# Optimization experiments

Hardware: AMD Instinct MI355X
Metric: run time of the kernel (lower is better)

Reference implementation:

```python
import jax, jax.numpy as jnp
import numpy as np

B, P, D = 256, 256, 514          # batch, num_patches (16^2), model_dim
H, HD = 8, 64                    # n_heads, head_dim ((D-2)//H)
SH = 256                         # shared_hidden = head_mlp_hidden_dims[0]
HH = 256                         # per-head hidden (head_mlp_hidden_dims[1])
DFF = 2048                       # ffn hidden
LH = 2 * SH                      # lat_modulator hidden = shared_hidden*2
LD = D - 2                       # learnable_dim

def gelu(x):
    return jax.nn.gelu(x, approximate=False)  # torch nn.GELU default is exact erf

def setup_inputs() -> dict:
    key = jax.random.key(0)
    ks = jax.random.split(key, 16)
    s = 0.02
    x = jax.random.normal(ks[0], (B, P, D), dtype=jnp.float32)
    # shared spatial layer: Linear(P -> SH), torch weight layout [out, in]
    Ws = jax.random.normal(ks[1], (SH, P), dtype=jnp.float32) * s
    bs = jax.random.normal(ks[2], (SH,), dtype=jnp.float32) * s
    # lat modulator: Linear(2 -> LH), GELU, Linear(LH -> 2*SH) with special init
    LW1 = jax.random.normal(ks[3], (LH, 2), dtype=jnp.float32) * s
    Lb1 = jax.random.normal(ks[4], (LH,), dtype=jnp.float32) * s
    LW2 = jnp.zeros((2 * SH, LH), dtype=jnp.float32)  # zeroed per module init
    Lb2 = jnp.concatenate([jnp.ones((SH,), jnp.float32), jnp.zeros((SH,), jnp.float32)])
    # per-head processing: Linear(SH->HH), GELU, Linear(HH->P), stacked over heads
    HW1 = jax.random.normal(ks[5], (H, HH, SH), dtype=jnp.float32) * s
    Hb1 = jax.random.normal(ks[6], (H, HH), dtype=jnp.float32) * s
    HW2 = jax.random.normal(ks[7], (H, P, HH), dtype=jnp.float32) * s
    Hb2 = jax.random.normal(ks[8], (H, P), dtype=jnp.float32) * s
    # ffn: Linear(D -> DFF) with last-2 input cols zeroed, GELU, Linear(DFF -> LD)
    FW1 = jax.random.normal(ks[9], (DFF, D), dtype=jnp.float32) * s
    FW1 = FW1.at[:, -2:].set(0.0)
    Fb1 = jax.random.normal(ks[10], (DFF,), dtype=jnp.float32) * s
    FW2 = jax.random.normal(ks[11], (LD, DFF), dtype=jnp.float32) * s
    Fb2 = jax.random.normal(ks[12], (LD,), dtype=jnp.float32) * s
    return dict(x=x, Ws=Ws, bs=bs, LW1=LW1, Lb1=Lb1, LW2=LW2, Lb2=Lb2,
                HW1=HW1, Hb1=Hb1, HW2=HW2, Hb2=Hb2,
                FW1=FW1, Fb1=Fb1, FW2=FW2, Fb2=Fb2)

def reference(x, Ws, bs, LW1, Lb1, LW2, Lb2, HW1, Hb1, HW2, Hb2, FW1, Fb1, FW2, Fb2):
    central = P // 2
    sc_central = x[:, central, -2:]          # [B, 2]
    sc_all = x[:, :, -2:]                    # [B, P, 2]
    x_learn = x[:, :, :-2]                   # [B, P, LD]
    x_res = x_learn
    # all heads at once: [B, P, H, HD] -> [B, H, HD, P]
    xh = x_learn.reshape(B, P, H, HD).transpose(0, 2, 3, 1)
    shared = jnp.einsum('bhdp,op->bhdo', xh, Ws) + bs   # [B, H, HD, SH]
    # FiLM params (loop-invariant in original, hoisted here)
    mod = gelu(sc_central @ LW1.T + Lb1) @ LW2.T + Lb2  # [B, 2*SH]
    gamma = mod[:, :SH][:, None, None, :]
    beta = mod[:, SH:][:, None, None, :]
    shared = shared * gamma + beta
    # per-head MLPs as grouped GEMMs
    h = gelu(jnp.einsum('bhdo,hko->bhdk', shared, HW1) + Hb1[None, :, None, :])
    out = jnp.einsum('bhdk,hpk->bhdp', h, HW2) + Hb2[None, :, None, :]  # [B,H,HD,P]
    x_learn = out.transpose(0, 3, 1, 2).reshape(B, P, LD) + x_res
    x_full = jnp.concatenate([x_learn, sc_all], axis=-1)  # [B, P, D]
    f = gelu(x_full @ FW1.T + Fb1) @ FW2.T + Fb2          # [B, P, LD]
    x_learn = f + x_learn
    return jnp.concatenate([x_learn, sc_all], axis=-1)
```

## Files before the change

kernel.cpp:

```cpp
#include <hip/hip_runtime.h>
#include <math.h>

typedef __attribute__((ext_vector_type(8))) __bf16 bf16x8;
typedef __attribute__((ext_vector_type(4))) float f32x4;
typedef __attribute__((ext_vector_type(2))) float f32x2;

#define DEV __device__ __forceinline__

typedef __attribute__((address_space(3))) unsigned int lds_u32;
typedef __attribute__((address_space(1))) unsigned int glb_u32;

DEV unsigned short f2bf(float f) {
    unsigned int u = __builtin_bit_cast(unsigned int, f);
    u += 0x7FFFu + ((u >> 16) & 1u);
    return (unsigned short)(u >> 16);
}
DEV float bf2f(unsigned short u) {
    unsigned int v = (unsigned int)u << 16;
    return __builtin_bit_cast(float, v);
}
DEV unsigned int pack2(float a, float b) {
    return (unsigned int)f2bf(a) | ((unsigned int)f2bf(b) << 16);
}
DEV float gelu_exact(float v) {
    return 0.5f * v * (1.0f + erff(v * 0.70710678118654752f));
}
DEV float gelu_fast(float x) {
    float z = 1.5957691216f * x + 0.0713548163f * x * x * x;
    float e = __expf(-z);
    return x * __builtin_amdgcn_rcpf(1.0f + e);
}

__global__ void cast_bf16_kernel(const float* __restrict__ src,
                                 unsigned short* __restrict__ dst, int n) {
    int i = blockIdx.x * 256 + threadIdx.x;
    if (i < n) dst[i] = f2bf(src[i]);
}

__global__ void cast_fw1_kernel(const float* __restrict__ src,
                                unsigned short* __restrict__ dst) {
    int i = blockIdx.x * 256 + threadIdx.x;
    if (i < 2048 * 512) {
        int row = i >> 9, k = i & 511;
        dst[i] = f2bf(src[row * 514 + k]);
    }
}

__global__ void gb_kernel(const float* __restrict__ x,
                          const float* __restrict__ LW1, const float* __restrict__ Lb1,
                          const float* __restrict__ LW2, const float* __restrict__ Lb2,
                          float* __restrict__ gb) {
    __shared__ float t[8][512];
    const int b0 = blockIdx.x * 8, tid = threadIdx.x;
    for (int idx = tid; idx < 8 * 512; idx += 256) {
        int bb = idx >> 9, j = idx & 511;
        float s0 = x[((size_t)(b0 + bb) * 256 + 128) * 514 + 512];
        float s1 = x[((size_t)(b0 + bb) * 256 + 128) * 514 + 513];
        t[bb][j] = gelu_exact(LW1[j * 2] * s0 + LW1[j * 2 + 1] * s1 + Lb1[j]);
    }
    __syncthreads();
    const int i = tid;
    float a0[8], a1[8];
    float l0 = Lb2[i], l1 = Lb2[i + 256];
    #pragma unroll
    for (int bb = 0; bb < 8; ++bb) { a0[bb] = l0; a1[bb] = l1; }
    for (int j = 0; j < 512; ++j) {
        float w0 = LW2[(size_t)i * 512 + j];
        float w1 = LW2[(size_t)(i + 256) * 512 + j];
        #pragma unroll
        for (int bb = 0; bb < 8; ++bb) {
            a0[bb] += w0 * t[bb][j];
            a1[bb] += w1 * t[bb][j];
        }
    }
    #pragma unroll
    for (int bb = 0; bb < 8; ++bb) {
        gb[(size_t)(b0 + bb) * 512 + i] = a0[bb];
        gb[(size_t)(b0 + bb) * 512 + i + 256] = a1[bb];
    }
}

__global__ void sc_copy_kernel(const float* __restrict__ x, float* __restrict__ out,
                               float* __restrict__ scbuf) {
    size_t idx = (size_t)blockIdx.x * 256 + threadIdx.x;
    size_t off = idx * 514 + 512;
    f32x2 v = *(const f32x2*)(x + off);
    *(f32x2*)(out + off) = v;
    *(f32x2*)(scbuf + idx * 2) = v;
}

#define MPAD 264

__global__ __launch_bounds__(256, 2) void mixer_kernel(
    const float* __restrict__ x, const float* __restrict__ bs,
    const float* __restrict__ Hb1, const float* __restrict__ Hb2,
    const unsigned short* __restrict__ Wsb,
    const unsigned short* __restrict__ HW1b,
    const unsigned short* __restrict__ HW2b,
    const float* __restrict__ gb,
    float* __restrict__ out,
    unsigned short* __restrict__ Xb) {
    __shared__ __attribute__((aligned(16))) char smem[33792 + 34816];
    unsigned short* XT = (unsigned short*)smem;
    unsigned short* S = (unsigned short*)(smem + 33792);
    unsigned short* ST = S;

    const int bid = blockIdx.x;
    const int b = bid >> 3;
    const int h = bid & 7;
    const int tid = threadIdx.x;
    const int lane = tid & 63;
    const int w = tid >> 6;
    const int l15 = lane & 15;
    const int l4 = lane >> 4;

    {
        const int c = lane;
        const float* xp = x + ((size_t)b * 256) * 514 + (size_t)h * 64 + c;
        for (int i = 0; i < 32; ++i) {
            int p = (i * 4 + w) * 2;
            float v0 = xp[(size_t)p * 514];
            float v1 = xp[(size_t)(p + 1) * 514];
            *(unsigned int*)&XT[c * MPAD + p] = pack2(v0, v1);
        }
    }
    __syncthreads();

    f32x4 acc[4][4];

    #pragma unroll
    for (int mt = 0; mt < 4; ++mt)
        #pragma unroll
        for (int nt = 0; nt < 4; ++nt) acc[mt][nt] = 0.f;
    {
        bf16x8 bnx[4];
        #pragma unroll
        for (int nt = 0; nt < 4; ++nt)
            bnx[nt] = *(const bf16x8*)(Wsb + (size_t)(w * 64 + nt * 16 + l15) * 256 + l4 * 8);
        for (int kc = 0; kc < 8; ++kc) {
            bf16x8 bcur[4];
            #pragma unroll
            for (int nt = 0; nt < 4; ++nt) bcur[nt] = bnx[nt];
            if (kc < 7) {
                #pragma unroll
                for (int nt = 0; nt < 4; ++nt)
                    bnx[nt] = *(const bf16x8*)(Wsb + (size_t)(w * 64 + nt * 16 + l15) * 256 + (kc + 1) * 32 + l4 * 8);
            }
            #pragma unroll
            for (int mt = 0; mt < 4; ++mt) {
                bf16x8 afr = *(const bf16x8*)&XT[(mt * 16 + l15) * MPAD + kc * 32 + l4 * 8];
                #pragma unroll
                for (int nt = 0; nt < 4; ++nt)
                    acc[mt][nt] = __builtin_amdgcn_mfma_f32_16x16x32_bf16(afr, bcur[nt], acc[mt][nt], 0, 0, 0);
            }
        }
    }
    #pragma unroll
    for (int nt = 0; nt < 4; ++nt) {
        int o = w * 64 + nt * 16 + l15;
        float bsv = bs[o];
        float g = gb[(size_t)b * 512 + o];
        float be = gb[(size_t)b * 512 + 256 + o];
        #pragma unroll
        for (int mt = 0; mt < 4; ++mt)
            #pragma unroll
            for (int r = 0; r < 4; ++r) {
                int c = mt * 16 + l4 * 4 + r;
                S[c * MPAD + o] = f2bf((acc[mt][nt][r] + bsv) * g + be);
            }
    }
    __syncthreads();

    const unsigned short* W2p = HW1b + (size_t)h * 65536;
    #pragma unroll
    for (int mt = 0; mt < 4; ++mt)
        #pragma unroll
        for (int nt = 0; nt < 4; ++nt) acc[mt][nt] = 0.f;
    {
        bf16x8 bnx[4];
        #pragma unroll
        for (int nt = 0; nt < 4; ++nt)
            bnx[nt] = *(const bf16x8*)(W2p + (size_t)(w * 64 + nt * 16 + l15) * 256 + l4 * 8);
        for (int kc = 0; kc < 8; ++kc) {
            bf16x8 bcur[4];
            #pragma unroll
            for (int nt = 0; nt < 4; ++nt) bcur[nt] = bnx[nt];
            if (kc < 7) {
                #pragma unroll
                for (int nt = 0; nt < 4; ++nt)
                    bnx[nt] = *(const bf16x8*)(W2p + (size_t)(w * 64 + nt * 16 + l15) * 256 + (kc + 1) * 32 + l4 * 8);
            }
            #pragma unroll
            for (int mt = 0; mt < 4; ++mt) {
                bf16x8 afr = *(const bf16x8*)&S[(mt * 16 + l15) * MPAD + kc * 32 + l4 * 8];
                #pragma unroll
                for (int nt = 0; nt < 4; ++nt)
                    acc[mt][nt] = __builtin_amdgcn_mfma_f32_16x16x32_bf16(afr, bcur[nt], acc[mt][nt], 0, 0, 0);
            }
        }
    }
    #pragma unroll
    for (int nt = 0; nt < 4; ++nt) {
        int kk = w * 64 + nt * 16 + l15;
        float hb = Hb1[(size_t)h * 256 + kk];
        #pragma unroll
        for (int mt = 0; mt < 4; ++mt)
            #pragma unroll
            for (int r = 0; r < 4; ++r) {
                int c = mt * 16 + l4 * 4 + r;
                XT[c * MPAD + kk] = f2bf(gelu_fast(acc[mt][nt][r] + hb));
            }
    }
    __syncthreads();

    const unsigned short* W3p = HW2b + (size_t)h * 65536;
    #pragma unroll
    for (int mt = 0; mt < 4; ++mt)
        #pragma unroll
        for (int nt = 0; nt < 4; ++nt) acc[mt][nt] = 0.f;
    {
        bf16x8 bnx[4];
        #pragma unroll
        for (int nt = 0; nt < 4; ++nt)
            bnx[nt] = *(const bf16x8*)(W3p + (size_t)(w * 64 + nt * 16 + l15) * 256 + l4 * 8);
        for (int kc = 0; kc < 8; ++kc) {
            bf16x8 bcur[4];
            #pragma unroll
            for (int nt = 0; nt < 4; ++nt) bcur[nt] = bnx[nt];
            if (kc < 7) {
                #pragma unroll
                for (int nt = 0; nt < 4; ++nt)
                    bnx[nt] = *(const bf16x8*)(W3p + (size_t)(w * 64 + nt * 16 + l15) * 256 + (kc + 1) * 32 + l4 * 8);
            }
            #pragma unroll
            for (int mt = 0; mt < 4; ++mt) {
                bf16x8 afr = *(const bf16x8*)&XT[(mt * 16 + l15) * MPAD + kc * 32 + l4 * 8];
                #pragma unroll
                for (int nt = 0; nt < 4; ++nt)
                    acc[mt][nt] = __builtin_amdgcn_mfma_f32_16x16x32_bf16(afr, bcur[nt], acc[mt][nt], 0, 0, 0);
            }
        }
    }
    #pragma unroll
    for (int nt = 0; nt < 4; ++nt) {
        int p = w * 64 + nt * 16 + l15;
        float hb = Hb2[(size_t)h * 256 + p];
        #pragma unroll
        for (int mt = 0; mt < 4; ++mt) {
            ushort4 uv;
            uv.x = f2bf(acc[mt][nt][0] + hb);
            uv.y = f2bf(acc[mt][nt][1] + hb);
            uv.z = f2bf(acc[mt][nt][2] + hb);
            uv.w = f2bf(acc[mt][nt][3] + hb);
            *(ushort4*)(ST + p * 68 + mt * 16 + l4 * 4) = uv;
        }
    }
    __syncthreads();

    #pragma unroll
    for (int s = 0; s < 16; ++s) {
        int row = s * 16 + w * 4 + l4;
        ushort4 u = *(const ushort4*)(ST + row * 68 + l15 * 4);
        const float* xr = x + ((size_t)(b * 256 + row)) * 514 + h * 64 + l15 * 4;
        f32x2 xa = *(const f32x2*)xr;
        f32x2 xc = *(const f32x2*)(xr + 2);
        float o0 = bf2f(u.x) + xa.x;
        float o1 = bf2f(u.y) + xa.y;
        float o2 = bf2f(u.z) + xc.x;
        float o3 = bf2f(u.w) + xc.y;
        float* orow = out + ((size_t)(b * 256 + row)) * 514 + h * 64 + l15 * 4;
        f32x2 w0; w0.x = o0; w0.y = o1;
        f32x2 w1; w1.x = o2; w1.y = o3;
        *(f32x2*)orow = w0;
        *(f32x2*)(orow + 2) = w1;
        ushort4 xo;
        xo.x = f2bf(o0); xo.y = f2bf(o1); xo.z = f2bf(o2); xo.w = f2bf(o3);
        *(ushort4*)(Xb + ((size_t)(b * 256 + row)) * 512 + h * 64 + l15 * 4) = xo;
    }
}

DEV void stage_half(const unsigned short* g, size_t gstride, int row0, int k0,
                    char* half_base, int w, int lane) {
    const int slot = lane & 7;
    const int r8 = lane >> 3;
    const int swz = (slot ^ r8) * 16;
    #pragma unroll
    for (int i = 0; i < 2; ++i) {
        int chunk = w * 2 + i;
        int row = chunk * 8 + r8;
        const char* src = (const char*)(g + (size_t)(row0 + row) * gstride + k0) + swz;
        __builtin_amdgcn_global_load_lds((const glb_u32*)src,
                                         (lds_u32*)(half_base + chunk * 1024), 16, 0, 0);
    }
}

DEV void gemm8_loop(const unsigned short* A, size_t sA,
                    const unsigned short* B, size_t sB,
                    int m0, int n0, int NT,
                    char* A0, char* A1, char* B0, char* B1,
                    int w, int lane, int l15, int l4,
                    f32x4 (&acc)[2][16]) {
    stage_half(A, sA, m0, 0, A0, w, lane);
    stage_half(A, sA, m0 + 128, 0, A0 + 16384, w, lane);
    stage_half(B, sB, n0, 0, B0, w, lane);
    stage_half(B, sB, n0 + 128, 0, B0 + 16384, w, lane);
    asm volatile("s_waitcnt vmcnt(2)" ::: "memory");
    __builtin_amdgcn_s_barrier();
    __builtin_amdgcn_sched_barrier(0);

    for (int t = 0; t < NT; ++t) {
        const char* Ac = (t & 1) ? A1 : A0;
        const char* Bc = (t & 1) ? B1 : B0;
        char* An = (t & 1) ? A0 : A1;
        char* Bn = (t & 1) ? B0 : B1;
        const int kn = (t + 1) * 64;
        const bool more = (t + 1 < NT);
        const bool last = (t == NT - 1);
        #pragma unroll
        for (int q = 0; q < 4; ++q) {
            bf16x8 af[2][2], bf[2][4];
            #pragma unroll
            for (int kk = 0; kk < 2; ++kk) {
                #pragma unroll
                for (int mt = 0; mt < 2; ++mt) {
                    int row = w * 32 + mt * 16 + l15;
                    af[kk][mt] = *(const bf16x8*)(Ac + row * 128 + ((kk * 64 + l4 * 16) ^ ((row & 7) << 4)));
                }
                #pragma unroll
                for (int nt = 0; nt < 4; ++nt) {
                    int row = q * 64 + nt * 16 + l15;
                    bf[kk][nt] = *(const bf16x8*)(Bc + row * 128 + ((kk * 64 + l4 * 16) ^ ((row & 7) << 4)));
                }
            }
            if (more) {
                if (q == 0) stage_half(A, sA, m0, kn, An, w, lane);
                if (q == 1) stage_half(A, sA, m0 + 128, kn, An + 16384, w, lane);
                if (q == 2) stage_half(B, sB, n0, kn, Bn, w, lane);
                if (q == 3) stage_half(B, sB, n0 + 128, kn, Bn + 16384, w, lane);
            }
            if (q == 1) {
                if (last) asm volatile("s_waitcnt vmcnt(0)" ::: "memory");
                else      asm volatile("s_waitcnt vmcnt(4)" ::: "memory");
            }
            if (q == 3) asm volatile("s_waitcnt vmcnt(2)" ::: "memory");
            __builtin_amdgcn_s_barrier();
            __builtin_amdgcn_sched_barrier(0);
            __builtin_amdgcn_s_setprio(1);
            #pragma unroll
            for (int kk = 0; kk < 2; ++kk)
                #pragma unroll
                for (int mt = 0; mt < 2; ++mt)
                    #pragma unroll
                    for (int nt = 0; nt < 4; ++nt)
                        acc[mt][q * 4 + nt] = __builtin_amdgcn_mfma_f32_16x16x32_bf16(
                            af[kk][mt], bf[kk][nt], acc[mt][q * 4 + nt], 0, 0, 0);
            __builtin_amdgcn_s_setprio(0);
            __builtin_amdgcn_sched_barrier(0);
            __builtin_amdgcn_s_barrier();
        }
    }
}

__global__ __launch_bounds__(512, 1) void gemm1_kernel(
    const unsigned short* __restrict__ A,
    const unsigned short* __restrict__ B,
    const float* __restrict__ Fb1,
    const float* __restrict__ FW1,
    const float* __restrict__ scbuf,
    long pass_m0,
    unsigned short* __restrict__ G) {
    __shared__ __attribute__((aligned(16))) char smem[131072];

    const int nwg = gridDim.x;
    const int cpx = nwg >> 3;
    const int bid = (blockIdx.x & 7) * cpx + (blockIdx.x >> 3);
    const int m0 = (bid >> 3) * 256;
    const int n0 = (bid & 7) * 256;
    const int tid = threadIdx.x;
    const int lane = tid & 63;
    const int w = tid >> 6;
    const int l15 = lane & 15;
    const int l4 = lane >> 4;

    f32x4 acc[2][16];
    #pragma unroll
    for (int mt = 0; mt < 2; ++mt)
        #pragma unroll
        for (int nt = 0; nt < 16; ++nt) acc[mt][nt] = 0.f;

    gemm8_loop(A, 512, B, 512, m0, n0, 8,
               smem, smem + 32768, smem + 65536, smem + 98304,
               w, lane, l15, l4, acc);

    f32x2 scp[2][4];
    #pragma unroll
    for (int mt = 0; mt < 2; ++mt)
        #pragma unroll
        for (int r = 0; r < 4; ++r) {
            long rowg = pass_m0 + m0 + w * 32 + mt * 16 + l4 * 4 + r;
            scp[mt][r] = *(const f32x2*)(scbuf + rowg * 2);
        }
    #pragma unroll
    for (int ntg = 0; ntg < 16; ++ntg) {
        int n = n0 + ntg * 16 + l15;
        float fb = Fb1[n];
        float w512 = FW1[(size_t)n * 514 + 512];
        float w513 = FW1[(size_t)n * 514 + 513];
        #pragma unroll
        for (int mt = 0; mt < 2; ++mt)
            #pragma unroll
            for (int r = 0; r < 4; ++r) {
                long row = m0 + w * 32 + mt * 16 + l4 * 4 + r;
                float v = acc[mt][ntg][r] + fb + scp[mt][r].x * w512 + scp[mt][r].y * w513;
                G[row * 2048 + n] = f2bf(gelu_fast(v));
            }
    }
}

__global__ __launch_bounds__(512, 1) void gemm2_kernel(
    const unsigned short* __restrict__ A,
    const unsigned short* __restrict__ B,
    const float* __restrict__ Fb2,
    long pass_m0,
    float* __restrict__ io) {
    __shared__ __attribute__((aligned(16))) char smem[131072];

    const int nwg = gridDim.x;
    const int cpx = nwg >> 3;
    const int bid = (blockIdx.x & 7) * cpx + (blockIdx.x >> 3);
    const int m0 = (bid >> 1) * 256;
    const int n0 = (bid & 1) * 256;
    const int tid = threadIdx.x;
    const int lane = tid & 63;
    const int w = tid >> 6;
    const int l15 = lane & 15;
    const int l4 = lane >> 4;

    f32x4 acc[2][16];
    #pragma unroll
    for (int mt = 0; mt < 2; ++mt)
        #pragma unroll
        for (int nt = 0; nt < 16; ++nt) acc[mt][nt] = 0.f;

    gemm8_loop(A, 2048, B, 2048, m0, n0, 32,
               smem, smem + 32768, smem + 65536, smem + 98304,
               w, lane, l15, l4, acc);

    #pragma unroll
    for (int ntg = 0; ntg < 16; ++ntg) {
        int n = n0 + ntg * 16 + l15;
        float fb = Fb2[n];
        #pragma unroll
        for (int mt = 0; mt < 2; ++mt)
            #pragma unroll
            for (int r = 0; r < 4; ++r) {
                long rowg = pass_m0 + m0 + w * 32 + mt * 16 + l4 * 4 + r;
                float* p = io + rowg * 514 + n;
                *p = acc[mt][ntg][r] + fb + *p;
            }
    }
}

extern "C" void kernel_launch(void* const* d_in, const int* in_sizes, int n_in,
                              void* d_out, int out_size, void* d_ws, size_t ws_size,
                              hipStream_t stream) {
    const float* x = (const float*)d_in[0];
    const float* Ws = (const float*)d_in[1];
    const float* bs = (const float*)d_in[2];
    const float* LW1 = (const float*)d_in[3];
    const float* Lb1 = (const float*)d_in[4];
    const float* LW2 = (const float*)d_in[5];
    const float* Lb2 = (const float*)d_in[6];
    const float* HW1 = (const float*)d_in[7];
    const float* Hb1 = (const float*)d_in[8];
    const float* HW2 = (const float*)d_in[9];
    const float* Hb2 = (const float*)d_in[10];
    const float* FW1 = (const float*)d_in[11];
    const float* Fb1 = (const float*)d_in[12];
    const float* FW2 = (const float*)d_in[13];
    const float* Fb2 = (const float*)d_in[14];
    float* out = (float*)d_out;

    char* ws = (char*)d_ws;
    unsigned short* Wsb = (unsigned short*)(ws);
    unsigned short* HW1b = (unsigned short*)(ws + 131072);
    unsigned short* HW2b = (unsigned short*)(ws + 1179648);
    unsigned short* FW1b = (unsigned short*)(ws + 2228224);
    unsigned short* FW2b = (unsigned short*)(ws + 4325376);
    float* gb = (float*)(ws + 6422528);
    float* scbuf = (float*)(ws + 6946816);
    unsigned short* Xb = (unsigned short*)(ws + 7471104);
    unsigned short* Gbuf = (unsigned short*)(ws + 7471104 + 67108864);

    const size_t fixed = 7471104 + 67108864;
    int npass = 32;
    for (int np = 1; np <= 32; np *= 2) {
        if (fixed + (size_t)268435456 / np <= ws_size) { npass = np; break; }
    }
    const long Mtot = 65536;
    const long Mp = Mtot / npass;

    cast_bf16_kernel<<<256, 256, 0, stream>>>(Ws, Wsb, 65536);
    cast_bf16_kernel<<<2048, 256, 0, stream>>>(HW1, HW1b, 524288);
    cast_bf16_kernel<<<2048, 256, 0, stream>>>(HW2, HW2b, 524288);
    cast_bf16_kernel<<<4096, 256, 0, stream>>>(FW2, FW2b, 1048576);
    cast_fw1_kernel<<<4096, 256, 0, stream>>>(FW1, FW1b);
    gb_kernel<<<32, 256, 0, stream>>>(x, LW1, Lb1, LW2, Lb2, gb);
    sc_copy_kernel<<<256, 256, 0, stream>>>(x, out, scbuf);

    mixer_kernel<<<2048, 256, 0, stream>>>(x, bs, Hb1, Hb2, Wsb, HW1b, HW2b, gb, out, Xb);

    for (int p = 0; p < npass; ++p) {
        long m0 = (long)p * Mp;
        gemm1_kernel<<<(int)(Mp / 256) * 8, 512, 0, stream>>>(
            Xb + m0 * 512, FW1b, Fb1, FW1, scbuf, m0, Gbuf);
        gemm2_kernel<<<(int)(Mp / 256) * 2, 512, 0, stream>>>(
            Gbuf, FW2b, Fb2, m0, out);
    }
}
```

Baseline: 665.1 us.

## Restructure FFN GEMM warp tiling to 2x4 layout with LDS-staged epilogue

Replaces the 8x1 warp layout (each warp 32 rows by 256 cols) with a 2x4 layout (each warp 128 rows by 64 cols). This raises register reuse of the A and B fragments and uses one barrier per k-tile instead of four. Staging of the next tile is issued at the start of each tile, followed by a full vmcnt wait. The gemm1 epilogue now writes GELU outputs to LDS and stores coalesced 16-byte rows to G instead of scattered 2-byte stores. The host now forces at least two passes, trading some launch overhead for a smaller G buffer footprint, possibly for L2/MALL locality.

```diff
diff --git a/kernel.cpp b/kernel.cpp
--- a/kernel.cpp
+++ b/kernel.cpp
@@ -294,70 +294,75 @@
     }
 }
 
-DEV void gemm8_loop(const unsigned short* A, size_t sA,
-                    const unsigned short* B, size_t sB,
-                    int m0, int n0, int NT,
-                    char* A0, char* A1, char* B0, char* B1,
-                    int w, int lane, int l15, int l4,
-                    f32x4 (&acc)[2][16]) {
-    stage_half(A, sA, m0, 0, A0, w, lane);
-    stage_half(A, sA, m0 + 128, 0, A0 + 16384, w, lane);
-    stage_half(B, sB, n0, 0, B0, w, lane);
-    stage_half(B, sB, n0 + 128, 0, B0 + 16384, w, lane);
-    asm volatile("s_waitcnt vmcnt(2)" ::: "memory");
+DEV void stage4(const unsigned short* A, size_t sA, int m0,
+                const unsigned short* B, size_t sB, int n0, int k0,
+                char* Abuf, char* Bbuf, int w, int lane) {
+    stage_half(A, sA, m0, k0, Abuf, w, lane);
+    stage_half(A, sA, m0 + 128, k0, Abuf + 16384, w, lane);
+    stage_half(B, sB, n0, k0, Bbuf, w, lane);
+    stage_half(B, sB, n0 + 128, k0, Bbuf + 16384, w, lane);
+}
+
+DEV void tile_body(const unsigned short* A, size_t sA, int m0,
+                   const unsigned short* B, size_t sB, int n0,
+                   char* smem, int cb, int kn, bool more,
+                   int vA0, int vA1, int vB0, int vB1,
+                   int w, int lane, f32x4 (&acc)[8][4]) {
+    if (more) {
+        int nb = 32768 - cb;
+        stage4(A, sA, m0, B, sB, n0, kn, smem + nb, smem + 65536 + nb, w, lane);
+    }
+    __builtin_amdgcn_s_setprio(1);
+    #pragma unroll
+    for (int kk = 0; kk < 2; ++kk) {
+        const int vA = kk ? vA1 : vA0;
+        const int vB = kk ? vB1 : vB0;
+        bf16x8 bf[4];
+        #pragma unroll
+        for (int nf = 0; nf < 4; ++nf)
+            bf[nf] = *(const bf16x8*)(smem + vB + cb + nf * 2048);
+        #pragma unroll
+        for (int mh = 0; mh < 2; ++mh) {
+            bf16x8 af[4];
+            #pragma unroll
+            for (int mf = 0; mf < 4; ++mf)
+                af[mf] = *(const bf16x8*)(smem + vA + cb + mh * 8192 + mf * 2048);
+            #pragma unroll
+            for (int mf = 0; mf < 4; ++mf)
+                #pragma unroll
+                for (int nf = 0; nf < 4; ++nf)
+                    acc[mh * 4 + mf][nf] = __builtin_amdgcn_mfma_f32_16x16x32_bf16(
+                        af[mf], bf[nf], acc[mh * 4 + mf][nf], 0, 0, 0);
+        }
+    }
+    __builtin_amdgcn_s_setprio(0);
+    if (more) asm volatile("s_waitcnt vmcnt(0)" ::: "memory");
     __builtin_amdgcn_s_barrier();
-    __builtin_amdgcn_sched_barrier(0);
-
-    for (int t = 0; t < NT; ++t) {
-        const char* Ac = (t & 1) ? A1 : A0;
-        const char* Bc = (t & 1) ? B1 : B0;
-        char* An = (t & 1) ? A0 : A1;
-        char* Bn = (t & 1) ? B0 : B1;
-        const int kn = (t + 1) * 64;
-        const bool more = (t + 1 < NT);
-        const bool last = (t == NT - 1);
-        #pragma unroll
-        for (int q = 0; q < 4; ++q) {
-            bf16x8 af[2][2], bf[2][4];
-            #pragma unroll
-            for (int kk = 0; kk < 2; ++kk) {
-                #pragma unroll
-                for (int mt = 0; mt < 2; ++mt) {
-                    int row = w * 32 + mt * 16 + l15;
-                    af[kk][mt] = *(const bf16x8*)(Ac + row * 128 + ((kk * 64 + l4 * 16) ^ ((row & 7) << 4)));
-                }
-                #pragma unroll
-                for (int nt = 0; nt < 4; ++nt) {
-                    int row = q * 64 + nt * 16 + l15;
-                    bf[kk][nt] = *(const bf16x8*)(Bc + row * 128 + ((kk * 64 + l4 * 16) ^ ((row & 7) << 4)));
-                }
-            }
-            if (more) {
-                if (q == 0) stage_half(A, sA, m0, kn, An, w, lane);
-                if (q == 1) stage_half(A, sA, m0 + 128, kn, An + 16384, w, lane);
-                if (q == 2) stage_half(B, sB, n0, kn, Bn, w, lane);
-                if (q == 3) stage_half(B, sB, n0 + 128, kn, Bn + 16384, w, lane);
-            }
-            if (q == 1) {
-                if (last) asm volatile("s_waitcnt vmcnt(0)" ::: "memory");
-                else      asm volatile("s_waitcnt vmcnt(4)" ::: "memory");
-            }
-            if (q == 3) asm volatile("s_waitcnt vmcnt(2)" ::: "memory");
-            __builtin_amdgcn_s_barrier();
-            __builtin_amdgcn_sched_barrier(0);
-            __builtin_amdgcn_s_setprio(1);
-            #pragma unroll
-            for (int kk = 0; kk < 2; ++kk)
-                #pragma unroll
-                for (int mt = 0; mt < 2; ++mt)
-                    #pragma unroll
-                    for (int nt = 0; nt < 4; ++nt)
-                        acc[mt][q * 4 + nt] = __builtin_amdgcn_mfma_f32_16x16x32_bf16(
-                            af[kk][mt], bf[kk][nt], acc[mt][q * 4 + nt], 0, 0, 0);
-            __builtin_amdgcn_s_setprio(0);
-            __builtin_amdgcn_sched_barrier(0);
-            __builtin_amdgcn_s_barrier();
-        }
+}
+
+DEV void gemm_loop(const unsigned short* A, size_t sA,
+                   const unsigned short* B, size_t sB,
+                   int m0, int n0, int NT,
+                   char* smem, int w, int lane, f32x4 (&acc)[8][4]) {
+    const int wm = w >> 2, wn = w & 3;
+    const int l15 = lane & 15, l4 = lane >> 4;
+    const int sw = (l15 & 7) << 4;
+    const int k0off = (l4 * 16) ^ sw;
+    const int k1off = (64 + l4 * 16) ^ sw;
+    const int aBase = (wm * 128 + l15) * 128;
+    const int bBase = 65536 + (wn * 64 + l15) * 128;
+    const int vA0 = aBase + k0off, vA1 = aBase + k1off;
+    const int vB0 = bBase + k0off, vB1 = bBase + k1off;
+
+    stage4(A, sA, m0, B, sB, n0, 0, smem, smem + 65536, w, lane);
+    asm volatile("s_waitcnt vmcnt(0)" ::: "memory");
+    __builtin_amdgcn_s_barrier();
+
+    for (int t = 0; t < NT; t += 2) {
+        tile_body(A, sA, m0, B, sB, n0, smem, 0, (t + 1) * 64, t + 1 < NT,
+                  vA0, vA1, vB0, vB1, w, lane, acc);
+        tile_body(A, sA, m0, B, sB, n0, smem, 32768, (t + 2) * 64, t + 2 < NT,
+                  vA0, vA1, vB0, vB1, w, lane, acc);
     }
 }
 
@@ -381,39 +386,57 @@
     const int w = tid >> 6;
     const int l15 = lane & 15;
     const int l4 = lane >> 4;
-
-    f32x4 acc[2][16];
-    #pragma unroll
-    for (int mt = 0; mt < 2; ++mt)
-        #pragma unroll
-        for (int nt = 0; nt < 16; ++nt) acc[mt][nt] = 0.f;
-
-    gemm8_loop(A, 512, B, 512, m0, n0, 8,
-               smem, smem + 32768, smem + 65536, smem + 98304,
-               w, lane, l15, l4, acc);
-
-    f32x2 scp[2][4];
-    #pragma unroll
-    for (int mt = 0; mt < 2; ++mt)
-        #pragma unroll
-        for (int r = 0; r < 4; ++r) {
-            long rowg = pass_m0 + m0 + w * 32 + mt * 16 + l4 * 4 + r;
-            scp[mt][r] = *(const f32x2*)(scbuf + rowg * 2);
-        }
-    #pragma unroll
-    for (int ntg = 0; ntg < 16; ++ntg) {
-        int n = n0 + ntg * 16 + l15;
-        float fb = Fb1[n];
-        float w512 = FW1[(size_t)n * 514 + 512];
-        float w513 = FW1[(size_t)n * 514 + 513];
-        #pragma unroll
-        for (int mt = 0; mt < 2; ++mt)
-            #pragma unroll
-            for (int r = 0; r < 4; ++r) {
-                long row = m0 + w * 32 + mt * 16 + l4 * 4 + r;
-                float v = acc[mt][ntg][r] + fb + scp[mt][r].x * w512 + scp[mt][r].y * w513;
-                G[row * 2048 + n] = f2bf(gelu_fast(v));
-            }
+    const int wm = w >> 2, wn = w & 3;
+
+    f32x4 acc[8][4];
+    #pragma unroll
+    for (int mf = 0; mf < 8; ++mf)
+        #pragma unroll
+        for (int nf = 0; nf < 4; ++nf) acc[mf][nf] = 0.f;
+
+    gemm_loop(A, 512, B, 512, m0, n0, 8, smem, w, lane, acc);
+
+    float fb[4], wa[4], wb[4];
+    #pragma unroll
+    for (int nf = 0; nf < 4; ++nf) {
+        int n = n0 + wn * 64 + nf * 16 + l15;
+        fb[nf] = Fb1[n];
+        wa[nf] = FW1[(size_t)n * 514 + 512];
+        wb[nf] = FW1[(size_t)n * 514 + 513];
+    }
+    unsigned short* LT = (unsigned short*)smem;
+    #pragma unroll
+    for (int ph = 0; ph < 2; ++ph) {
+        if (wm == ph) {
+            #pragma unroll
+            for (int mfg = 0; mfg < 8; ++mfg) {
+                f32x2 sc[4];
+                #pragma unroll
+                for (int r = 0; r < 4; ++r) {
+                    long rowg = pass_m0 + m0 + ph * 128 + mfg * 16 + l4 * 4 + r;
+                    sc[r] = *(const f32x2*)(scbuf + rowg * 2);
+                }
+                #pragma unroll
+                for (int nf = 0; nf < 4; ++nf)
+                    #pragma unroll
+                    for (int r = 0; r < 4; ++r) {
+                        float v = acc[mfg][nf][r] + fb[nf] + sc[r].x * wa[nf] + sc[r].y * wb[nf];
+                        int rl = mfg * 16 + l4 * 4 + r;
+                        LT[rl * 264 + wn * 64 + nf * 16 + l15] = f2bf(gelu_fast(v));
+                    }
+            }
+        }
+        __syncthreads();
+        {
+            const int row16 = tid >> 5, col16 = tid & 31;
+            #pragma unroll
+            for (int sp = 0; sp < 8; ++sp) {
+                int row = sp * 16 + row16;
+                uint4 d = *(const uint4*)((const char*)smem + row * 528 + col16 * 16);
+                *(uint4*)(G + ((size_t)(m0 + ph * 128 + row)) * 2048 + n0 + col16 * 8) = d;
+            }
+        }
+        __syncthreads();
     }
 }
 
@@ -435,28 +458,27 @@
     const int w = tid >> 6;
     const int l15 = lane & 15;
     const int l4 = lane >> 4;
-
-    f32x4 acc[2][16];
-    #pragma unroll
-    for (int mt = 0; mt < 2; ++mt)
-        #pragma unroll
-        for (int nt = 0; nt < 16; ++nt) acc[mt][nt] = 0.f;
-
-    gemm8_loop(A, 2048, B, 2048, m0, n0, 32,
-               smem, smem + 32768, smem + 65536, smem + 98304,
-               w, lane, l15, l4, acc);
-
-    #pragma unroll
-    for (int ntg = 0; ntg < 16; ++ntg) {
-        int n = n0 + ntg * 16 + l15;
-        float fb = Fb2[n];
-        #pragma unroll
-        for (int mt = 0; mt < 2; ++mt)
+    const int wm = w >> 2, wn = w & 3;
+
+    f32x4 acc[8][4];
+    #pragma unroll
+    for (int mf = 0; mf < 8; ++mf)
+        #pragma unroll
+        for (int nf = 0; nf < 4; ++nf) acc[mf][nf] = 0.f;
+
+    gemm_loop(A, 2048, B, 2048, m0, n0, 32, smem, w, lane, acc);
+
+    #pragma unroll
+    for (int nf = 0; nf < 4; ++nf) {
+        int n = n0 + wn * 64 + nf * 16 + l15;
+        float fbv = Fb2[n];
+        #pragma unroll
+        for (int mfg = 0; mfg < 8; ++mfg)
             #pragma unroll
             for (int r = 0; r < 4; ++r) {
-                long rowg = pass_m0 + m0 + w * 32 + mt * 16 + l4 * 4 + r;
+                long rowg = pass_m0 + m0 + wm * 128 + mfg * 16 + l4 * 4 + r;
                 float* p = io + rowg * 514 + n;
-                *p = acc[mt][ntg][r] + fb + *p;
+                *p = acc[mfg][nf][r] + fbv + *p;
             }
     }
 }
@@ -494,7 +516,7 @@
 
     const size_t fixed = 7471104 + 67108864;
     int npass = 32;
-    for (int np = 1; np <= 32; np *= 2) {
+    for (int np = 2; np <= 32; np *= 2) {
         if (fixed + (size_t)268435456 / np <= ws_size) { npass = np; break; }
     }
     const long Mtot = 65536;
```

Measured after the change: 714.7 us. +7.5%, slower.
